# Optimization experiments

Hardware: AMD Instinct MI355X
Metric: run time of the kernel (lower is better)

Reference implementation:

```python
import jax, jax.numpy as jnp
import numpy as np

B, L, V, D = 8, 2048, 1024, 512  # batch, seq (max_len), vocab_size (input feat), embedding_dim

def setup_inputs() -> dict:
    key = jax.random.key(0)
    kx, kq, kk, kv = jax.random.split(key, 4)
    scale = 1.0 / np.sqrt(V)
    return {
        "x": jax.random.normal(kx, (B, L, V), dtype=jnp.float32),
        "Wq": jax.random.uniform(kq, (D, V), dtype=jnp.float32, minval=-scale, maxval=scale),
        "Wk": jax.random.uniform(kk, (D, V), dtype=jnp.float32, minval=-scale, maxval=scale),
        "Wv": jax.random.uniform(kv, (D, V), dtype=jnp.float32, minval=-scale, maxval=scale),
    }

def reference(x, Wq, Wk, Wv):
    # nn.Linear without bias: y = x @ W.T
    q = jnp.einsum('blv,dv->bld', x, Wq)
    k = jnp.einsum('blv,dv->bld', x, Wk)
    v = jnp.einsum('blv,dv->bld', x, Wv)
    scores = jnp.einsum('bqd,bkd->bqk', q, k) / jnp.sqrt(jnp.float32(D))
    attn = jax.nn.softmax(scores, axis=2)
    return jnp.einsum('bqk,bkd->bqd', attn, v)
```

## Files before the change

kernel.cpp:

```cpp
#include <hip/hip_runtime.h>
#include <cstdint>
#include <cstddef>


typedef __attribute__((ext_vector_type(8))) __bf16 bf16x8;
typedef __attribute__((ext_vector_type(4))) float f32x4;
typedef __attribute__((ext_vector_type(4))) unsigned short ushort4v;
typedef __attribute__((ext_vector_type(4))) unsigned int uint4v;

__device__ __forceinline__ unsigned short f2bf(float f) {
  unsigned u = __float_as_uint(f);
  return (unsigned short)((u + 0x7fffu + ((u >> 16) & 1u)) >> 16);
}

__device__ __forceinline__ void async_load16(const unsigned short* g, unsigned short* l) {
  __builtin_amdgcn_global_load_lds(
      (__attribute__((address_space(1))) void*)(g),
      (__attribute__((address_space(3))) void*)(l), 16, 0, 0);
}

__global__ __launch_bounds__(256) void cvt_all(
    const float* __restrict__ x, const float* __restrict__ Wq,
    const float* __restrict__ Wk, const float* __restrict__ Wv,
    unsigned short* __restrict__ xb, unsigned short* __restrict__ wf) {
  int tid = threadIdx.x;
  for (int u0 = blockIdx.x; u0 < 17920; u0 += 2048) {
    const float* src;
    unsigned short* dst;
    int i;
    if (u0 < 16384) {
      i = (u0 * 256 + tid) * 4;
      src = x; dst = xb;
    } else {
      int bx = u0 - 16384;
      src = (bx < 512) ? Wq : (bx < 1024) ? Wk : Wv;
      int seg = (bx < 512) ? 0 : (bx < 1024) ? 1 : 2;
      i = ((bx & 511) * 256 + tid) * 4;
      dst = wf + seg * 524288;
    }
    float4 v = *(const float4*)(src + i);
    ushort4v o;
    o.x = f2bf(v.x); o.y = f2bf(v.y); o.z = f2bf(v.z); o.w = f2bf(v.w);
    *(ushort4v*)(dst + i) = o;
  }
}

template <int NT>
__device__ __forceinline__ void core8p(
    const unsigned short* __restrict__ A, const unsigned short* __restrict__ B,
    int ldA, int ldB, unsigned short* smem, int tid, f32x4 (&acc)[4][4]) {
  const int lane = tid & 63, wid = tid >> 6;
  const int wm = wid & 3, wn = wid >> 2;
  const int cl = lane & 15, g = lane >> 4;
  const int r0 = tid >> 3;
  const int cs8 = ((tid & 7) ^ (r0 & 7)) * 8;

  #pragma unroll
  for (int p = 0; p < 4; ++p)
    async_load16(&A[(size_t)(p * 64 + r0) * ldA + cs8], &smem[(p * 512 + tid) * 8]);
  #pragma unroll
  for (int p = 0; p < 2; ++p)
    async_load16(&B[(size_t)(p * 64 + r0) * ldB + cs8], &smem[16384 + (p * 512 + tid) * 8]);
  #pragma unroll
  for (int p = 0; p < 4; ++p)
    async_load16(&A[(size_t)(p * 64 + r0) * ldA + 64 + cs8], &smem[24576 + (p * 512 + tid) * 8]);
  #pragma unroll
  for (int p = 0; p < 2; ++p)
    async_load16(&B[(size_t)(p * 64 + r0) * ldB + 64 + cs8], &smem[40960 + (p * 512 + tid) * 8]);
  asm volatile("s_waitcnt vmcnt(6)" ::: "memory");
  __builtin_amdgcn_s_barrier();

  int cur = 0;
  for (int t = 0; t < NT; ++t) {
    unsigned short* bufc = smem + cur * 24576;
    int nb = cur + 2; if (nb >= 3) nb -= 3;
    unsigned short* bufn = smem + nb * 24576;
    const bool st = (t + 2 < NT);
    const int k2 = (t + 2) * 64;

    #pragma unroll
    for (int kh = 0; kh < 2; ++kh) {
      bf16x8 a4[4], b4[4];
      #pragma unroll
      for (int mt = 0; mt < 4; ++mt) {
        int rr = wm * 64 + mt * 16 + cl;
        a4[mt] = *(const bf16x8*)&bufc[(rr * 8 + ((kh * 4 + g) ^ (rr & 7))) * 8];
      }
      #pragma unroll
      for (int nt = 0; nt < 4; ++nt) {
        int rr = wn * 64 + nt * 16 + cl;
        b4[nt] = *(const bf16x8*)&bufc[16384 + (rr * 8 + ((kh * 4 + g) ^ (rr & 7))) * 8];
      }
      if (kh == 0) {
        if (st) {
          #pragma unroll
          for (int p = 0; p < 4; ++p)
            async_load16(&A[(size_t)(p * 64 + r0) * ldA + k2 + cs8],
                         &bufn[(p * 512 + tid) * 8]);
        }
      } else {
        if (st) {
          #pragma unroll
          for (int p = 0; p < 2; ++p)
            async_load16(&B[(size_t)(p * 64 + r0) * ldB + k2 + cs8],
                         &bufn[16384 + (p * 512 + tid) * 8]);
          asm volatile("s_waitcnt vmcnt(6)" ::: "memory");
        } else if (t + 1 < NT) {
          asm volatile("s_waitcnt vmcnt(0)" ::: "memory");
        }
      }
      __builtin_amdgcn_s_barrier();
      asm volatile("s_waitcnt lgkmcnt(0)" ::: "memory");
      __builtin_amdgcn_sched_barrier(0);
      __builtin_amdgcn_s_setprio(1);
      #pragma unroll
      for (int mt = 0; mt < 4; ++mt)
        #pragma unroll
        for (int nt = 0; nt < 4; ++nt)
          acc[mt][nt] = __builtin_amdgcn_mfma_f32_16x16x32_bf16(
              a4[mt], b4[nt], acc[mt][nt], 0, 0, 0);
      __builtin_amdgcn_s_setprio(0);
      __builtin_amdgcn_s_barrier();
    }
    cur = cur + 1; if (cur == 3) cur = 0;
  }
}

__global__ __launch_bounds__(512, 2) void gemm_qkv8(
    const unsigned short* __restrict__ A0,
    const unsigned short* __restrict__ Bw,
    unsigned short* __restrict__ qk,
    unsigned short* __restrict__ vT) {
  extern __shared__ __align__(16) unsigned short smem[];
  const int tid = threadIdx.x;
  int flat = blockIdx.x;
  int sub = flat >> 3;
  int bxp = sub % 12;
  int byp = (flat & 7) * 8 + sub / 12;
  const unsigned short* A = A0 + (size_t)byp * 256 * 1024;
  const unsigned short* B = Bw + (size_t)bxp * 128 * 1024;

  f32x4 acc[4][4] = {};
  core8p<16>(A, B, 1024, 1024, smem, tid, acc);

  const int lane = tid & 63, wid = tid >> 6;
  const int wm = wid & 3, wn = wid >> 2, cl = lane & 15, g = lane >> 4;

  if (bxp < 8) {
    unsigned short* Cc = qk + (size_t)byp * 256 * 1024 + (size_t)bxp * 128;
    #pragma unroll
    for (int mt = 0; mt < 4; ++mt)
      #pragma unroll
      for (int nt = 0; nt < 4; ++nt) {
        int col = wn * 64 + nt * 16 + cl;
        int row0 = wm * 64 + mt * 16 + g * 4;
        #pragma unroll
        for (int j = 0; j < 4; ++j)
          Cc[(size_t)(row0 + j) * 1024 + col] = f2bf(acc[mt][nt][j]);
      }
  } else {
    int nvx = bxp - 8;
    #pragma unroll
    for (int mt = 0; mt < 4; ++mt)
      #pragma unroll
      for (int nt = 0; nt < 4; ++nt) {
        int d = nvx * 128 + wn * 64 + nt * 16 + cl;
        int grow0 = byp * 256 + wm * 64 + mt * 16 + g * 4;
        int b = grow0 >> 11, l0 = grow0 & 2047;
        ushort4v o;
        o.x = f2bf(acc[mt][nt][0]); o.y = f2bf(acc[mt][nt][1]);
        o.z = f2bf(acc[mt][nt][2]); o.w = f2bf(acc[mt][nt][3]);
        *(ushort4v*)&vT[(size_t)b * 1048576 + (size_t)d * 2048 + l0] = o;
      }
  }
}

__global__ __launch_bounds__(256) void gemm_exp(
    const unsigned short* __restrict__ qk,
    unsigned short* __restrict__ S) {
  const float scale = 0.044194173824159216f;
  __shared__ unsigned short sA[128 * 64];
  __shared__ unsigned short sB[128 * 64];
  const int tid = threadIdx.x;
  const int lane = tid & 63, wid = tid >> 6;
  const int wm = wid & 1, wn = wid >> 1;
  const int cl = lane & 15, g = lane >> 4;

  int flat = blockIdx.x + (blockIdx.y << 4) + (blockIdx.z << 8);
  int z = flat & 7, rem = flat >> 3;
  int bxp = rem & 15, byp = rem >> 4;

  const unsigned short* A  = qk + (size_t)z * 2097152 + (size_t)byp * 128 * 1024;
  const unsigned short* Bk = qk + 512 + (size_t)z * 2097152 + (size_t)bxp * 128 * 1024;

  f32x4 acc[4][4] = {};

  for (int k0 = 0; k0 < 512; k0 += 64) {
    __syncthreads();
    #pragma unroll
    for (int p = 0; p < 4; ++p) {
      int u = p * 256 + tid;
      int r = u >> 3, cs = (u & 7) ^ (r & 7);
      async_load16(&A[(size_t)r * 1024 + k0 + cs * 8], &sA[u * 8]);
      async_load16(&Bk[(size_t)r * 1024 + k0 + cs * 8], &sB[u * 8]);
    }
    __syncthreads();

    bf16x8 aF[4][2], bF[4][2];
    #pragma unroll
    for (int t = 0; t < 4; ++t)
      #pragma unroll
      for (int kh = 0; kh < 2; ++kh) {
        int ra = wm * 64 + t * 16 + cl;
        aF[t][kh] = *(const bf16x8*)&sA[(ra * 8 + ((kh * 4 + g) ^ (ra & 7))) * 8];
        int rb = wn * 64 + t * 16 + cl;
        bF[t][kh] = *(const bf16x8*)&sB[(rb * 8 + ((kh * 4 + g) ^ (rb & 7))) * 8];
      }
    #pragma unroll
    for (int mt = 0; mt < 4; ++mt)
      #pragma unroll
      for (int nt = 0; nt < 4; ++nt)
        #pragma unroll
        for (int kh = 0; kh < 2; ++kh)
          acc[mt][nt] = __builtin_amdgcn_mfma_f32_16x16x32_bf16(
              aF[mt][kh], bF[nt][kh], acc[mt][nt], 0, 0, 0);
  }

  unsigned short* Cc = S + (size_t)z * 4194304 +
                       (size_t)byp * 128 * 2048 + (size_t)bxp * 128;
  #pragma unroll
  for (int mt = 0; mt < 4; ++mt)
    #pragma unroll
    for (int nt = 0; nt < 4; ++nt) {
      int col = wn * 64 + nt * 16 + cl;
      int row0 = wm * 64 + mt * 16 + g * 4;
      #pragma unroll
      for (int j = 0; j < 4; ++j)
        Cc[(size_t)(row0 + j) * 2048 + col] =
            f2bf(__expf(acc[mt][nt][j] * scale));
    }
}

__global__ __launch_bounds__(256) void gemm_pv(
    const unsigned short* __restrict__ P, const unsigned short* __restrict__ vT,
    float* __restrict__ out) {
  __shared__ unsigned short sA[128 * 64];
  __shared__ unsigned short sB[128 * 64];
  __shared__ float rs[128];
  const int tid = threadIdx.x;
  const int lane = tid & 63, wid = tid >> 6;
  const int wm = wid & 1, wn = wid >> 1;
  const int cl = lane & 15, g = lane >> 4;

  int flat = blockIdx.x + (blockIdx.y << 2) + (blockIdx.z << 6);
  int z = flat & 7, rem = flat >> 3;
  int bxp = rem & 3, byp = rem >> 2;

  const int m0 = byp * 128, n0 = bxp * 128;
  const unsigned short* A  = P + (size_t)z * 4194304 + (size_t)m0 * 2048;
  const unsigned short* Bv = vT + (size_t)z * 1048576 + (size_t)n0 * 2048;

  f32x4 acc[4][4] = {};
  float rsum[4] = {0.f, 0.f, 0.f, 0.f};

  for (int k0 = 0; k0 < 2048; k0 += 64) {
    __syncthreads();
    #pragma unroll
    for (int p = 0; p < 4; ++p) {
      int u = p * 256 + tid;
      int r = u >> 3, cs = (u & 7) ^ (r & 7);
      async_load16(&A[(size_t)r * 2048 + k0 + cs * 8], &sA[u * 8]);
      async_load16(&Bv[(size_t)r * 2048 + k0 + cs * 8], &sB[u * 8]);
    }
    __syncthreads();

    bf16x8 aF[4][2], bF[4][2];
    #pragma unroll
    for (int t = 0; t < 4; ++t)
      #pragma unroll
      for (int kh = 0; kh < 2; ++kh) {
        int ra = wm * 64 + t * 16 + cl;
        aF[t][kh] = *(const bf16x8*)&sA[(ra * 8 + ((kh * 4 + g) ^ (ra & 7))) * 8];
        int rb = wn * 64 + t * 16 + cl;
        bF[t][kh] = *(const bf16x8*)&sB[(rb * 8 + ((kh * 4 + g) ^ (rb & 7))) * 8];
      }
    #pragma unroll
    for (int t = 0; t < 4; ++t)
      #pragma unroll
      for (int kh = 0; kh < 2; ++kh) {
        uint4v u = __builtin_bit_cast(uint4v, aF[t][kh]);
        #pragma unroll
        for (int q = 0; q < 4; ++q)
          rsum[t] += __uint_as_float(u[q] << 16) +
                     __uint_as_float(u[q] & 0xffff0000u);
      }
    #pragma unroll
    for (int mt = 0; mt < 4; ++mt)
      #pragma unroll
      for (int nt = 0; nt < 4; ++nt)
        #pragma unroll
        for (int kh = 0; kh < 2; ++kh)
          acc[mt][nt] = __builtin_amdgcn_mfma_f32_16x16x32_bf16(
              aF[mt][kh], bF[nt][kh], acc[mt][nt], 0, 0, 0);
  }

  #pragma unroll
  for (int mt = 0; mt < 4; ++mt) {
    float v = rsum[mt];
    v += __shfl_xor(v, 16, 64);
    v += __shfl_xor(v, 32, 64);
    if (wn == 0 && lane < 16) rs[wm * 64 + mt * 16 + lane] = v;
  }
  __syncthreads();

  #pragma unroll
  for (int mt = 0; mt < 4; ++mt) {
    int row0l = wm * 64 + mt * 16 + g * 4;
    float inv[4];
    #pragma unroll
    for (int j = 0; j < 4; ++j) inv[j] = __builtin_amdgcn_rcpf(rs[row0l + j]);
    #pragma unroll
    for (int nt = 0; nt < 4; ++nt) {
      int col = n0 + wn * 64 + nt * 16 + cl;
      float* op = out + ((size_t)z * 2048 + m0 + row0l) * 512 + col;
      #pragma unroll
      for (int j = 0; j < 4; ++j)
        op[(size_t)j * 512] = acc[mt][nt][j] * inv[j];
    }
  }
}

extern "C" void kernel_launch(void* const* d_in, const int* in_sizes, int n_in,
                              void* d_out, int out_size, void* d_ws, size_t ws_size,
                              hipStream_t stream) {
  const float* x  = (const float*)d_in[0];
  const float* Wq = (const float*)d_in[1];
  const float* Wk = (const float*)d_in[2];
  const float* Wv = (const float*)d_in[3];
  float* out = (float*)d_out;
  char* ws = (char*)d_ws;

  unsigned short* xb = (unsigned short*)ws;
  unsigned short* S  = (unsigned short*)ws;
  unsigned short* wf = (unsigned short*)(ws + 33554432);
  unsigned short* qk = (unsigned short*)(ws + 67108864);
  unsigned short* vT = (unsigned short*)(ws + 100663296);

  static bool inited = false;
  if (!inited) {
    hipFuncSetAttribute((const void*)gemm_qkv8,
                        hipFuncAttributeMaxDynamicSharedMemorySize, 147456);
    inited = true;
  }

  hipLaunchKernelGGL(cvt_all, dim3(2048), dim3(256), 0, stream,
                     x, Wq, Wk, Wv, xb, wf);

  hipLaunchKernelGGL(gemm_qkv8, dim3(768), dim3(512), 147456, stream,
                     xb, wf, qk, vT);

  hipLaunchKernelGGL(gemm_exp, dim3(16, 16, 8), dim3(256), 0, stream, qk, S);

  hipLaunchKernelGGL(gemm_pv, dim3(4, 16, 8), dim3(256), 0, stream, S, vT, out);

  (void)in_sizes; (void)n_in; (void)out_size; (void)ws_size;
}
```

Measured before the change: 251.2 us.

## Fuse QK^T exp and PV GEMMs into a single flash-style attention kernel

Replaces the separate score-exp kernel and the P·V kernel with one fused kernel. Each block keeps a 64-query Q tile in registers, streams K and V tiles through shared memory, computes exp scores into LDS and accumulates P·V and the row sums on the fly. This avoids writing and re-reading the full bf16 B×L×L score matrix in HBM and saves one launch. In exchange it launches only 256 blocks of 512 threads, so each block runs a long serial loop with many barriers, and it still does no running max subtraction.

```diff
diff --git a/kernel.cpp b/kernel.cpp
--- a/kernel.cpp
+++ b/kernel.cpp
@@ -175,159 +175,144 @@
   }
 }
 
-__global__ __launch_bounds__(256) void gemm_exp(
+__global__ __launch_bounds__(512, 2) void fused_sv(
     const unsigned short* __restrict__ qk,
-    unsigned short* __restrict__ S) {
-  const float scale = 0.044194173824159216f;
-  __shared__ unsigned short sA[128 * 64];
-  __shared__ unsigned short sB[128 * 64];
+    const unsigned short* __restrict__ vT,
+    float* __restrict__ out) {
+  extern __shared__ __align__(16) unsigned short smem[];
   const int tid = threadIdx.x;
   const int lane = tid & 63, wid = tid >> 6;
-  const int wm = wid & 1, wn = wid >> 1;
+  const int wq = wid & 3, wk = wid >> 2;
   const int cl = lane & 15, g = lane >> 4;
 
-  int flat = blockIdx.x + (blockIdx.y << 4) + (blockIdx.z << 8);
-  int z = flat & 7, rem = flat >> 3;
-  int bxp = rem & 15, byp = rem >> 4;
-
-  const unsigned short* A  = qk + (size_t)z * 2097152 + (size_t)byp * 128 * 1024;
-  const unsigned short* Bk = qk + 512 + (size_t)z * 2097152 + (size_t)bxp * 128 * 1024;
-
+  int flat = blockIdx.x;
+  int b = flat & 7, qp = flat >> 3;
+  const unsigned short* Q = qk + (size_t)b * 2097152 + (size_t)qp * 64 * 1024;
+  const unsigned short* K = qk + (size_t)b * 2097152 + 512;
+  const unsigned short* V = vT + (size_t)b * 1048576;
+  float* O = out + ((size_t)b * 2048 + (size_t)qp * 64) * 512;
+
+  #pragma unroll
+  for (int p = 0; p < 8; ++p) {
+    int u = p * 512 + tid;
+    int r = u >> 6, c = u & 63;
+    async_load16(&Q[(size_t)r * 1024 + (c ^ (r & 7)) * 8], &smem[u * 8]);
+  }
+  __syncthreads();
+  bf16x8 qf[16];
+  {
+    int row = wq * 16 + cl;
+    #pragma unroll
+    for (int s = 0; s < 16; ++s)
+      qf[s] = *(const bf16x8*)&smem[(row * 64 + ((s * 4 + g) ^ (row & 7))) * 8];
+  }
+  __syncthreads();
+
+  float* rs2 = (float*)(smem + 45056);
   f32x4 acc[4][4] = {};
-
-  for (int k0 = 0; k0 < 512; k0 += 64) {
+  float rsumP[4] = {0.f, 0.f, 0.f, 0.f};
+  const float scale = 0.044194173824159216f;
+
+  for (int kt = 0; kt < 32; ++kt) {
+    f32x4 Sacc[2] = {};
+    #pragma unroll
+    for (int dc = 0; dc < 4; ++dc) {
+      __syncthreads();
+      #pragma unroll
+      for (int p = 0; p < 2; ++p) {
+        int u = p * 512 + tid;
+        int r = u >> 4, c = u & 15;
+        async_load16(&K[(size_t)(kt * 64 + r) * 1024 + dc * 128 + (c ^ (r & 7)) * 8],
+                     &smem[u * 8]);
+      }
+      if (dc == 0) {
+        #pragma unroll
+        for (int p = 0; p < 8; ++p) {
+          int u = p * 64 + lane;
+          int r = u >> 3, c = u & 7;
+          async_load16(&V[(size_t)(wid * 64 + r) * 2048 + kt * 64 + (c ^ (r & 7)) * 8],
+                       &smem[8192 + wid * 4096 + u * 8]);
+        }
+      }
+      __syncthreads();
+      #pragma unroll
+      for (int s = 0; s < 4; ++s) {
+        bf16x8 kf[2];
+        #pragma unroll
+        for (int nt = 0; nt < 2; ++nt) {
+          int rr = wk * 32 + nt * 16 + cl;
+          kf[nt] = *(const bf16x8*)&smem[(rr * 16 + ((s * 4 + g) ^ (rr & 7))) * 8];
+        }
+        #pragma unroll
+        for (int nt = 0; nt < 2; ++nt)
+          Sacc[nt] = __builtin_amdgcn_mfma_f32_16x16x32_bf16(
+              qf[dc * 4 + s], kf[nt], Sacc[nt], 0, 0, 0);
+      }
+    }
+    #pragma unroll
+    for (int nt = 0; nt < 2; ++nt) {
+      int col = wk * 32 + nt * 16 + cl;
+      #pragma unroll
+      for (int j = 0; j < 4; ++j) {
+        float e = __expf(Sacc[nt][j] * scale);
+        rsumP[j] += e;
+        int row = wq * 16 + g * 4 + j;
+        smem[40960 + row * 64 + (((col >> 3) ^ (row & 7)) * 8) + (col & 7)] = f2bf(e);
+      }
+    }
     __syncthreads();
-    #pragma unroll
-    for (int p = 0; p < 4; ++p) {
-      int u = p * 256 + tid;
-      int r = u >> 3, cs = (u & 7) ^ (r & 7);
-      async_load16(&A[(size_t)r * 1024 + k0 + cs * 8], &sA[u * 8]);
-      async_load16(&Bk[(size_t)r * 1024 + k0 + cs * 8], &sB[u * 8]);
-    }
-    __syncthreads();
-
-    bf16x8 aF[4][2], bF[4][2];
-    #pragma unroll
-    for (int t = 0; t < 4; ++t)
-      #pragma unroll
-      for (int kh = 0; kh < 2; ++kh) {
-        int ra = wm * 64 + t * 16 + cl;
-        aF[t][kh] = *(const bf16x8*)&sA[(ra * 8 + ((kh * 4 + g) ^ (ra & 7))) * 8];
-        int rb = wn * 64 + t * 16 + cl;
-        bF[t][kh] = *(const bf16x8*)&sB[(rb * 8 + ((kh * 4 + g) ^ (rb & 7))) * 8];
-      }
-    #pragma unroll
-    for (int mt = 0; mt < 4; ++mt)
-      #pragma unroll
-      for (int nt = 0; nt < 4; ++nt)
-        #pragma unroll
-        for (int kh = 0; kh < 2; ++kh)
+    const unsigned short* vb = &smem[8192 + wid * 4096];
+    #pragma unroll
+    for (int ks = 0; ks < 2; ++ks) {
+      bf16x8 pf[4], vf[4];
+      #pragma unroll
+      for (int mt = 0; mt < 4; ++mt) {
+        int rr = mt * 16 + cl;
+        pf[mt] = *(const bf16x8*)&smem[40960 + rr * 64 + (((ks * 4 + g) ^ (rr & 7)) * 8)];
+      }
+      #pragma unroll
+      for (int nt = 0; nt < 4; ++nt) {
+        int rr = nt * 16 + cl;
+        vf[nt] = *(const bf16x8*)&vb[rr * 64 + (((ks * 4 + g) ^ (rr & 7)) * 8)];
+      }
+      #pragma unroll
+      for (int mt = 0; mt < 4; ++mt)
+        #pragma unroll
+        for (int nt = 0; nt < 4; ++nt)
           acc[mt][nt] = __builtin_amdgcn_mfma_f32_16x16x32_bf16(
-              aF[mt][kh], bF[nt][kh], acc[mt][nt], 0, 0, 0);
-  }
-
-  unsigned short* Cc = S + (size_t)z * 4194304 +
-                       (size_t)byp * 128 * 2048 + (size_t)bxp * 128;
+              pf[mt], vf[nt], acc[mt][nt], 0, 0, 0);
+    }
+  }
+
+  #pragma unroll
+  for (int j = 0; j < 4; ++j) {
+    float v = rsumP[j];
+    v += __shfl_xor(v, 1, 64);
+    v += __shfl_xor(v, 2, 64);
+    v += __shfl_xor(v, 4, 64);
+    v += __shfl_xor(v, 8, 64);
+    rsumP[j] = v;
+  }
+  __syncthreads();
+  if (cl == 0) {
+    #pragma unroll
+    for (int j = 0; j < 4; ++j)
+      rs2[wk * 64 + wq * 16 + g * 4 + j] = rsumP[j];
+  }
+  __syncthreads();
+
   #pragma unroll
   for (int mt = 0; mt < 4; ++mt)
     #pragma unroll
-    for (int nt = 0; nt < 4; ++nt) {
-      int col = wn * 64 + nt * 16 + cl;
-      int row0 = wm * 64 + mt * 16 + g * 4;
-      #pragma unroll
-      for (int j = 0; j < 4; ++j)
-        Cc[(size_t)(row0 + j) * 2048 + col] =
-            f2bf(__expf(acc[mt][nt][j] * scale));
-    }
-}
-
-__global__ __launch_bounds__(256) void gemm_pv(
-    const unsigned short* __restrict__ P, const unsigned short* __restrict__ vT,
-    float* __restrict__ out) {
-  __shared__ unsigned short sA[128 * 64];
-  __shared__ unsigned short sB[128 * 64];
-  __shared__ float rs[128];
-  const int tid = threadIdx.x;
-  const int lane = tid & 63, wid = tid >> 6;
-  const int wm = wid & 1, wn = wid >> 1;
-  const int cl = lane & 15, g = lane >> 4;
-
-  int flat = blockIdx.x + (blockIdx.y << 2) + (blockIdx.z << 6);
-  int z = flat & 7, rem = flat >> 3;
-  int bxp = rem & 3, byp = rem >> 2;
-
-  const int m0 = byp * 128, n0 = bxp * 128;
-  const unsigned short* A  = P + (size_t)z * 4194304 + (size_t)m0 * 2048;
-  const unsigned short* Bv = vT + (size_t)z * 1048576 + (size_t)n0 * 2048;
-
-  f32x4 acc[4][4] = {};
-  float rsum[4] = {0.f, 0.f, 0.f, 0.f};
-
-  for (int k0 = 0; k0 < 2048; k0 += 64) {
-    __syncthreads();
-    #pragma unroll
-    for (int p = 0; p < 4; ++p) {
-      int u = p * 256 + tid;
-      int r = u >> 3, cs = (u & 7) ^ (r & 7);
-      async_load16(&A[(size_t)r * 2048 + k0 + cs * 8], &sA[u * 8]);
-      async_load16(&Bv[(size_t)r * 2048 + k0 + cs * 8], &sB[u * 8]);
-    }
-    __syncthreads();
-
-    bf16x8 aF[4][2], bF[4][2];
-    #pragma unroll
-    for (int t = 0; t < 4; ++t)
-      #pragma unroll
-      for (int kh = 0; kh < 2; ++kh) {
-        int ra = wm * 64 + t * 16 + cl;
-        aF[t][kh] = *(const bf16x8*)&sA[(ra * 8 + ((kh * 4 + g) ^ (ra & 7))) * 8];
-        int rb = wn * 64 + t * 16 + cl;
-        bF[t][kh] = *(const bf16x8*)&sB[(rb * 8 + ((kh * 4 + g) ^ (rb & 7))) * 8];
-      }
-    #pragma unroll
-    for (int t = 0; t < 4; ++t)
-      #pragma unroll
-      for (int kh = 0; kh < 2; ++kh) {
-        uint4v u = __builtin_bit_cast(uint4v, aF[t][kh]);
-        #pragma unroll
-        for (int q = 0; q < 4; ++q)
-          rsum[t] += __uint_as_float(u[q] << 16) +
-                     __uint_as_float(u[q] & 0xffff0000u);
-      }
-    #pragma unroll
-    for (int mt = 0; mt < 4; ++mt)
-      #pragma unroll
-      for (int nt = 0; nt < 4; ++nt)
-        #pragma unroll
-        for (int kh = 0; kh < 2; ++kh)
-          acc[mt][nt] = __builtin_amdgcn_mfma_f32_16x16x32_bf16(
-              aF[mt][kh], bF[nt][kh], acc[mt][nt], 0, 0, 0);
-  }
-
-  #pragma unroll
-  for (int mt = 0; mt < 4; ++mt) {
-    float v = rsum[mt];
-    v += __shfl_xor(v, 16, 64);
-    v += __shfl_xor(v, 32, 64);
-    if (wn == 0 && lane < 16) rs[wm * 64 + mt * 16 + lane] = v;
-  }
-  __syncthreads();
-
-  #pragma unroll
-  for (int mt = 0; mt < 4; ++mt) {
-    int row0l = wm * 64 + mt * 16 + g * 4;
-    float inv[4];
-    #pragma unroll
-    for (int j = 0; j < 4; ++j) inv[j] = __builtin_amdgcn_rcpf(rs[row0l + j]);
-    #pragma unroll
-    for (int nt = 0; nt < 4; ++nt) {
-      int col = n0 + wn * 64 + nt * 16 + cl;
-      float* op = out + ((size_t)z * 2048 + m0 + row0l) * 512 + col;
-      #pragma unroll
-      for (int j = 0; j < 4; ++j)
-        op[(size_t)j * 512] = acc[mt][nt][j] * inv[j];
-    }
-  }
+    for (int j = 0; j < 4; ++j) {
+      int row = mt * 16 + g * 4 + j;
+      float inv = __builtin_amdgcn_rcpf(rs2[row] + rs2[64 + row]);
+      #pragma unroll
+      for (int nt = 0; nt < 4; ++nt) {
+        int d = wid * 64 + nt * 16 + cl;
+        O[(size_t)row * 512 + d] = acc[mt][nt][j] * inv;
+      }
+    }
 }
 
 extern "C" void kernel_launch(void* const* d_in, const int* in_sizes, int n_in,
@@ -341,7 +326,6 @@
   char* ws = (char*)d_ws;
 
   unsigned short* xb = (unsigned short*)ws;
-  unsigned short* S  = (unsigned short*)ws;
   unsigned short* wf = (unsigned short*)(ws + 33554432);
   unsigned short* qk = (unsigned short*)(ws + 67108864);
   unsigned short* vT = (unsigned short*)(ws + 100663296);
@@ -350,6 +334,8 @@
   if (!inited) {
     hipFuncSetAttribute((const void*)gemm_qkv8,
                         hipFuncAttributeMaxDynamicSharedMemorySize, 147456);
+    hipFuncSetAttribute((const void*)fused_sv,
+                        hipFuncAttributeMaxDynamicSharedMemorySize, 90624);
     inited = true;
   }
 
@@ -359,9 +345,8 @@
   hipLaunchKernelGGL(gemm_qkv8, dim3(768), dim3(512), 147456, stream,
                      xb, wf, qk, vT);
 
-  hipLaunchKernelGGL(gemm_exp, dim3(16, 16, 8), dim3(256), 0, stream, qk, S);
-
-  hipLaunchKernelGGL(gemm_pv, dim3(4, 16, 8), dim3(256), 0, stream, S, vT, out);
+  hipLaunchKernelGGL(fused_sv, dim3(256), dim3(512), 90624, stream,
+                     qk, vT, out);
 
   (void)in_sizes; (void)n_in; (void)out_size; (void)ws_size;
 }
```

Result: slower. 301.5 us (+20.0%).
